# Optimization experiments

Measured on AMD Instinct MI355X. Metric: run time of the kernel, lower is better.

The kernel has to match this reference:

```python
import jax, jax.numpy as jnp
import numpy as np

N, E, D, R, L = 100000, 800000, 64, 7, 3
HID, KH = D // 4, 32          # IEConv hidden = dims[i]//4, kernel_hidden_dim = 32
EDGE_DIM = 14
BN_EPS = 1e-5
LN_EPS = 1e-5


def _normalize(v, eps=1e-12):
    n = jnp.linalg.norm(v, axis=-1, keepdims=True)
    return v / jnp.maximum(n, eps)


def _bn(h, p):
    # eval-mode BatchNorm1d; p: [4, dim] = (gamma, beta, running_mean, running_var)
    return (h - p[2]) * jax.lax.rsqrt(p[3] + BN_EPS) * p[0] + p[1]


def setup_inputs() -> dict:
    key = jax.random.key(0)
    keys = iter(jax.random.split(key, 40))
    nk = lambda: next(keys)
    par = lambda shape, s=0.1: jax.random.normal(nk(), shape, jnp.float32) * s

    def bn_par(dim):
        g = 1.0 + 0.1 * jax.random.normal(nk(), (L, dim), jnp.float32)
        b = 0.1 * jax.random.normal(nk(), (L, dim), jnp.float32)
        m = 0.1 * jax.random.normal(nk(), (L, dim), jnp.float32)
        v = 0.5 + jax.random.uniform(nk(), (L, dim), jnp.float32)
        return jnp.stack([g, b, m, v], axis=1)  # [L,4,dim]

    inp = {
        "x": jax.random.normal(nk(), (N, D), jnp.float32),
        "pos": jax.random.normal(nk(), (N, 3), jnp.float32) * 10.0,
        "edge_index": jax.random.randint(nk(), (2, E), 0, N),
        "edge_relation": jax.random.randint(nk(), (E,), 0, R),
        # GeometricRelationalGraphConv params (per layer)
        "W_rel": par((L, R * D, D)), "b_rel": par((L, D)),
        "W_self": par((L, D, D)), "b_self": par((L, D)),
        # IEConvLayer params
        "W_l1": par((L, D, HID)), "b_l1": par((L, HID)),
        "W_k1": par((L, EDGE_DIM, KH)), "b_k1": par((L, KH)),
        "W_k2": par((L, KH, (HID + 1) * HID)), "b_k2": par((L, (HID + 1) * HID)),
        "W_l2": par((L, HID, D)), "b_l2": par((L, D)),
        "bn_in": bn_par(D), "bn_msg": bn_par(HID), "bn_upd": bn_par(HID), "bn_out": bn_par(D),
        "ln_g": 1.0 + 0.1 * jax.random.normal(nk(), (L, D), jnp.float32),
        "ln_b": 0.1 * jax.random.normal(nk(), (L, D), jnp.float32),
    }
    return inp


def _forward(x, pos, W_rel, b_rel, W_self, b_self, W_l1, b_l1, W_k1, b_k1,
             W_k2, b_k2, W_l2, b_l2, bn_in, bn_msg, bn_upd, bn_out, ln_g, ln_b,
             edge_index, edge_relation):
    node_in, node_out = edge_index[0], edge_index[1]
    # ---- get_ieconv_edge_feature ----
    ones3 = jnp.ones((1, 3), x.dtype)
    u = _normalize(jnp.concatenate([ones3, pos[1:] - pos[:-1]], axis=0))        # [N,3]
    b = _normalize(jnp.concatenate([u[:-1] - u[1:], ones3], axis=0))
    n = _normalize(jnp.concatenate([jnp.cross(u[:-1], u[1:]), ones3], axis=0))
    frame = jnp.stack([b, n, jnp.cross(b, n)], axis=-1)                          # [N,3,3]
    t = jnp.einsum('ejk,ej->ek', frame[node_in], pos[node_out] - pos[node_in])  # [E,3]
    r = jnp.sum(frame[node_in] * frame[node_out], axis=1)                        # [E,3]
    delta = (jnp.abs(node_in - node_out).astype(x.dtype) / 6.0)[:, None]         # atom2residue = arange
    edge_feat = jnp.concatenate(
        [t, r, delta, 1 - 2 * jnp.abs(t), 1 - 2 * jnp.abs(r), 1 - 2 * jnp.abs(delta)], axis=-1)  # [E,14]

    deg = jnp.maximum(
        jax.ops.segment_sum(jnp.ones_like(node_out, dtype=x.dtype), node_out, num_segments=N), 1.0)[:, None]
    seg = node_out * R + edge_relation
    h = x
    for i in range(L):
        # GeometricRelationalGraphConv: relation-bucketed scatter-sum, per-relation linear + self loop, relu
        upd = jax.ops.segment_sum(h[node_in], seg, num_segments=N * R).reshape(N, R * h.shape[-1])
        rel_out = jax.nn.relu(upd @ W_rel[i] + b_rel[i] + h @ W_self[i] + b_self[i])
        # IEConvLayer (eval mode, dropouts identity)
        li = jax.nn.relu(_bn(h, bn_in[i]))
        m = jax.nn.relu(_bn(li[node_in] @ W_l1[i] + b_l1[i], bn_msg[i]))         # [E,HID]
        ker = (jax.nn.relu(edge_feat @ W_k1[i] + b_k1[i]) @ W_k2[i] + b_k2[i]).reshape(-1, HID + 1, HID)
        m = jnp.einsum('ejk,ej->ek', ker[:, 1:, :], m) + ker[:, 0, :]            # per-edge kernel conv
        upd2 = jax.ops.segment_sum(m, node_out, num_segments=N) / deg            # scatter-mean
        upd2 = jax.nn.relu(_bn(upd2, bn_upd[i]))
        ie_out = _bn(upd2 @ W_l2[i] + b_l2[i], bn_out[i])
        hidden = rel_out + ie_out + h  # short_cut: shapes match at every layer
        mu = jnp.mean(hidden, axis=-1, keepdims=True)
        var = jnp.var(hidden, axis=-1, keepdims=True)
        h = (hidden - mu) * jax.lax.rsqrt(var + LN_EPS) * ln_g[i] + ln_b[i]
    return h


def reference(x, pos, edge_index, edge_relation, W_rel, b_rel, W_self, b_self,
              W_l1, b_l1, W_k1, b_k1, W_k2, b_k2, W_l2, b_l2,
              bn_in, bn_msg, bn_upd, bn_out, ln_g, ln_b):
    return _forward(x, pos, W_rel, b_rel, W_self, b_self, W_l1, b_l1, W_k1, b_k1,
                    W_k2, b_k2, W_l2, b_l2, bn_in, bn_msg, bn_upd, bn_out, ln_g, ln_b,
                    edge_index, edge_relation)
```

## Files before the change

### kernel.cpp

```cpp
#include <hip/hip_runtime.h>
#include <hip/hip_bf16.h>

typedef unsigned short u16;
typedef unsigned int   u32;

static const int Nn  = 100000;
static const int Ne  = 800000;
static const int Ll  = 3;
static const int SCAN_B = 98;

typedef short     short8  __attribute__((ext_vector_type(8)));
typedef float     floatx4 __attribute__((ext_vector_type(4)));

static const int H_CUM[19] = {
  0, 86016, 86208, 98496, 98688, 101760, 101808, 103152, 103248,
  129360, 130176, 133248, 133440, 134208, 134400, 134592, 135360, 135552, 135744
};
static const int H_SZ[18] = {
  86016, 192, 12288, 192, 3072, 48, 1344, 96,
  26112, 816, 3072, 192, 768, 192, 192, 768, 192, 192
};

union FU { u32 u; float f; };
__device__ __forceinline__ float b2f(u16 v) { FU x; x.u = ((u32)v) << 16; return x.f; }
__device__ __forceinline__ float lo2f(u32 w) { FU x; x.u = w << 16; return x.f; }
__device__ __forceinline__ float hi2f(u32 w) { FU x; x.u = w & 0xffff0000u; return x.f; }
__device__ __forceinline__ u16 f2b(float f) {
  FU x; x.f = f;
  u32 u = x.u;
  u32 r = (u + 0x7FFFu + ((u >> 16) & 1u)) >> 16;
  return (u16)r;
}
__device__ __forceinline__ u32 pk2(float a, float b) {
  __hip_bfloat162 h2 = __float22bfloat162_rn(make_float2(a, b));
  union { __hip_bfloat162 h; u32 u; } c; c.h = h2; return c.u;
}

__global__ void k_bnprep(const float* __restrict__ W, float* __restrict__ bnAB) {
  int idx = blockIdx.x * blockDim.x + threadIdx.x;
  if (idx >= 480) return;
  int i = idx / 160, d0 = idx % 160;
  const float* src; float* dstA; float* dstB; int dim, d;
  if (d0 < 64)       { d = d0;      src = W + 133440 + i * 256; dim = 64; dstA = bnAB + i*320 + 0;   dstB = bnAB + i*320 + 64;  }
  else if (d0 < 80)  { d = d0 - 64; src = W + 134208 + i * 64;  dim = 16; dstA = bnAB + i*320 + 128; dstB = bnAB + i*320 + 144; }
  else if (d0 < 96)  { d = d0 - 80; src = W + 134400 + i * 64;  dim = 16; dstA = bnAB + i*320 + 160; dstB = bnAB + i*320 + 176; }
  else               { d = d0 - 96; src = W + 134592 + i * 256; dim = 64; dstA = bnAB + i*320 + 192; dstB = bnAB + i*320 + 256; }
  float g = src[0*dim+d], b = src[1*dim+d], m = src[2*dim+d], v = src[3*dim+d];
  float A = g * rsqrtf(v + 1e-5f);
  float B = b - m * A;
  dstA[d] = A; dstB[d] = B;
}

__global__ void k_prep(const float* __restrict__ W, u16* __restrict__ BswG) {
  int i = blockIdx.x * 256 + threadIdx.x;
  if (i >= 3 * 8704) return;
  int layer = i / 8704, r = i % 8704;
  int jp = r / 512, l2 = r % 512;
  int lane = l2 / 8, j = l2 % 8;
  int q = (lane >> 4) * 8 + j, n = lane & 15;
  const float* Wk2 = W + 103248 + layer * 8704;
  BswG[i] = f2b(Wk2[q * 272 + jp * 16 + n]);
}

__global__ void k_prep2(const float* __restrict__ W, u16* __restrict__ B2) {
  int idx = blockIdx.x * 256 + threadIdx.x;
  if (idx >= 3 * 65536) return;
  int layer = idx >> 16, r = idx & 65535;
  int fr = r >> 9;
  int lane = (r >> 3) & 63, j = r & 7;
  int hl = fr & 1, ks = (fr >> 1) & 1, nt = (fr >> 2) & 3, nc = fr >> 4;
  int k = ks * 32 + (lane >> 4) * 8 + j;
  int g = nc * 64 + nt * 16 + (lane & 15);
  const float* Wrel  = W + layer * 28672;
  const float* Wself = W + 86208 + layer * 4096;
  float v = (g < 448) ? Wrel[((g >> 6) * 64 + k) * 64 + (g & 63)]
                      : Wself[k * 64 + (g - 448)];
  u16 hi = f2b(v);
  B2[idx] = hl ? f2b(v - b2f(hi)) : hi;
}

__global__ void k_prep3(const float* __restrict__ W, u16* __restrict__ Wk1f) {
  int idx = blockIdx.x * 256 + threadIdx.x;
  if (idx >= 3 * 2048) return;
  int layer = idx / 2048, r = idx % 2048;
  int kind = (r >> 10) & 1, nt = (r >> 9) & 1;
  int lane = (r >> 3) & 63, j = r & 7;
  int k = (lane >> 4) * 8 + j;
  int q = nt * 16 + (lane & 15);
  const float* Wk1 = W + 101808 + layer * 448;
  u16 out = 0;
  if (kind == 0) {
    if (k < 14)       out = f2b(Wk1[k * 32 + q]);
    else if (k < 28)  out = f2b(Wk1[(k - 14) * 32 + q]);
  } else {
    if (k < 14) {
      float w = Wk1[k * 32 + q];
      u16 hi = f2b(w);
      out = f2b(w - b2f(hi));
    }
  }
  Wk1f[idx] = out;
}

__global__ void k_u(const float* __restrict__ posf, float* __restrict__ u) {
  int i = blockIdx.x * blockDim.x + threadIdx.x;
  if (i >= Nn) return;
  float ux, uy, uz;
  if (i == 0) { ux = uy = uz = 0.57735026918962584f; }
  else {
    float vx = posf[i*3+0] - posf[(i-1)*3+0];
    float vy = posf[i*3+1] - posf[(i-1)*3+1];
    float vz = posf[i*3+2] - posf[(i-1)*3+2];
    float nrm = sqrtf(vx*vx + vy*vy + vz*vz);
    float inv = 1.0f / fmaxf(nrm, 1e-12f);
    ux = vx*inv; uy = vy*inv; uz = vz*inv;
  }
  u[i*3+0] = ux; u[i*3+1] = uy; u[i*3+2] = uz;
}

__global__ void k_frame(const float* __restrict__ u, float* __restrict__ frame) {
  int i = blockIdx.x * blockDim.x + threadIdx.x;
  if (i >= Nn) return;
  float bx, by, bz, nx, ny, nz;
  if (i < Nn - 1) {
    float ax = u[i*3+0], ay = u[i*3+1], az = u[i*3+2];
    float cx = u[(i+1)*3+0], cy = u[(i+1)*3+1], cz = u[(i+1)*3+2];
    float dx = ax-cx, dy = ay-cy, dz = az-cz;
    float n1 = sqrtf(dx*dx + dy*dy + dz*dz);
    float i1 = 1.0f / fmaxf(n1, 1e-12f);
    bx = dx*i1; by = dy*i1; bz = dz*i1;
    float qx = ay*cz - az*cy, qy = az*cx - ax*cz, qz = ax*cy - ay*cx;
    float n2 = sqrtf(qx*qx + qy*qy + qz*qz);
    float i2 = 1.0f / fmaxf(n2, 1e-12f);
    nx = qx*i2; ny = qy*i2; nz = qz*i2;
  } else {
    bx = by = bz = 0.57735026918962584f;
    nx = ny = nz = 0.57735026918962584f;
  }
  float ex = by*nz - bz*ny, ey = bz*nx - bx*nz, ez = bx*ny - by*nx;
  frame[i*9+0] = bx; frame[i*9+1] = nx; frame[i*9+2] = ex;
  frame[i*9+3] = by; frame[i*9+4] = ny; frame[i*9+5] = ey;
  frame[i*9+6] = bz; frame[i*9+7] = nz; frame[i*9+8] = ez;
}

__global__ void k_edge(const int* __restrict__ EI, const float* __restrict__ posf,
                       const float* __restrict__ frame,
                       float* __restrict__ t0, float* __restrict__ t1, float* __restrict__ t2,
                       float* __restrict__ r0, float* __restrict__ r1, float* __restrict__ r2,
                       int* __restrict__ cnt) {
  int e = blockIdx.x * 256 + threadIdx.x;
  int vin = EI[e], vout = EI[Ne + e];
  float fi[9], fo[9];
#pragma unroll
  for (int t = 0; t < 9; t++) fi[t] = frame[(size_t)vin*9 + t];
#pragma unroll
  for (int t = 0; t < 9; t++) fo[t] = frame[(size_t)vout*9 + t];
  float d0 = posf[vout*3+0] - posf[vin*3+0];
  float d1 = posf[vout*3+1] - posf[vin*3+1];
  float d2 = posf[vout*3+2] - posf[vin*3+2];
  float tt[3], rr[3];
#pragma unroll
  for (int k = 0; k < 3; k++) {
    tt[k] = fi[0*3+k]*d0 + fi[1*3+k]*d1 + fi[2*3+k]*d2;
    rr[k] = fi[0*3+k]*fo[0*3+k] + fi[1*3+k]*fo[1*3+k] + fi[2*3+k]*fo[2*3+k];
  }
  t0[e] = tt[0]; t1[e] = tt[1]; t2[e] = tt[2];
  r0[e] = rr[0]; r1[e] = rr[1]; r2[e] = rr[2];
  atomicAdd(&cnt[vout], 1);
}

__global__ __launch_bounds__(1024) void k_scan1(const int* __restrict__ cnt,
                                                int* __restrict__ locExc,
                                                int* __restrict__ btot) {
  __shared__ int sm[1024];
  int t = threadIdx.x, b = blockIdx.x;
  int i = b * 1024 + t;
  int v = (i < Nn) ? cnt[i] : 0;
  sm[t] = v;
  __syncthreads();
#pragma unroll
  for (int off = 1; off < 1024; off <<= 1) {
    int x = (t >= off) ? sm[t - off] : 0;
    __syncthreads();
    sm[t] += x;
    __syncthreads();
  }
  if (i < Nn) locExc[i] = sm[t] - v;
  if (t == 1023) btot[b] = sm[1023];
}

__global__ void k_scan2(const int* __restrict__ btot, int* __restrict__ boff,
                        int* __restrict__ rowptr) {
  if (threadIdx.x != 0 || blockIdx.x != 0) return;
  int run = 0;
  for (int b = 0; b < SCAN_B; b++) { boff[b] = run; run += btot[b]; }
  rowptr[Nn] = run;
}

__global__ void k_scan3(const int* __restrict__ cnt, const int* __restrict__ locExc,
                        const int* __restrict__ boff, int* __restrict__ rowptr,
                        float* __restrict__ deginv) {
  int i = blockIdx.x * blockDim.x + threadIdx.x;
  if (i >= Nn) return;
  rowptr[i] = locExc[i] + boff[i >> 10];
  int dv = cnt[i] > 1 ? cnt[i] : 1;
  deginv[i] = 1.0f / (float)dv;
}

__global__ void k_place(const int* __restrict__ EI, const int* __restrict__ EREL,
                        const int* __restrict__ rowptr,
                        int* __restrict__ fill, int* __restrict__ yidx,
                        int* __restrict__ inv) {
  int e = blockIdx.x * blockDim.x + threadIdx.x;
  if (e >= Ne) return;
  int vout = EI[Ne + e];
  int p = atomicAdd(&fill[vout], 1);
  int slot = rowptr[vout] + p;
  inv[e] = slot;
  yidx[slot] = EI[e] * 448 + EREL[e] * 64;
}

__global__ __launch_bounds__(256) void k_rel2(
    const float* __restrict__ h, const u16* __restrict__ Bsw,
    const float* __restrict__ brel, const float* __restrict__ bself,
    u16* __restrict__ Y, u16* __restrict__ S) {
  __shared__ uint4 bs4[1024];
  int tid = threadIdx.x;
  int w = tid >> 6, lane = tid & 63;
  int kq = lane >> 4, cl = lane & 15;
  int nb0 = blockIdx.x * 64;
  int anode = nb0 + w * 16 + cl;
  union U { uint4 u; short8 v; };

  uint4 Ah[2], Al[2];
#pragma unroll
  for (int ks = 0; ks < 2; ks++) {
    float p[8] = {0.f,0.f,0.f,0.f,0.f,0.f,0.f,0.f};
    if (anode < Nn) {
      const float4* hp = (const float4*)(h + (size_t)anode * 64 + ks * 32 + kq * 8);
      float4 q0 = hp[0], q1 = hp[1];
      p[0]=q0.x; p[1]=q0.y; p[2]=q0.z; p[3]=q0.w;
      p[4]=q1.x; p[5]=q1.y; p[6]=q1.z; p[7]=q1.w;
    }
    u32 hw[4], lw[4];
#pragma unroll
    for (int t = 0; t < 4; t++) {
      u16 ha = f2b(p[2*t]), hb = f2b(p[2*t+1]);
      hw[t] = (u32)ha | ((u32)hb << 16);
      lw[t] = pk2(p[2*t] - b2f(ha), p[2*t+1] - b2f(hb));
    }
    Ah[ks] = make_uint4(hw[0], hw[1], hw[2], hw[3]);
    Al[ks] = make_uint4(lw[0], lw[1], lw[2], lw[3]);
  }

  for (int nc = 0; nc < 8; nc++) {
    if (nc) __syncthreads();
    const uint4* src = (const uint4*)(Bsw + nc * 8192);
#pragma unroll
    for (int i = 0; i < 4; i++) bs4[tid + i * 256] = src[tid + i * 256];
    __syncthreads();

    floatx4 acc[4];
#pragma unroll
    for (int nt = 0; nt < 4; nt++) acc[nt] = (floatx4){0.f, 0.f, 0.f, 0.f};
#pragma unroll
    for (int nt = 0; nt < 4; nt++) {
#pragma unroll
      for (int ks = 0; ks < 2; ks++) {
        U bh, bl, ah, al;
        bh.u = bs4[((nt*2 + ks)*2 + 0)*64 + lane];
        bl.u = bs4[((nt*2 + ks)*2 + 1)*64 + lane];
        ah.u = Ah[ks]; al.u = Al[ks];
        acc[nt] = __builtin_amdgcn_mfma_f32_16x16x32_bf16(ah.v, bh.v, acc[nt], 0, 0, 0);
        acc[nt] = __builtin_amdgcn_mfma_f32_16x16x32_bf16(al.v, bh.v, acc[nt], 0, 0, 0);
        acc[nt] = __builtin_amdgcn_mfma_f32_16x16x32_bf16(ah.v, bl.v, acc[nt], 0, 0, 0);
      }
    }
    if (nc < 7) {
#pragma unroll
      for (int nt = 0; nt < 4; nt++) {
#pragma unroll
        for (int reg = 0; reg < 4; reg++) {
          int node = nb0 + w * 16 + kq * 4 + reg;
          if (node < Nn)
            Y[(size_t)node * 448 + nc * 64 + nt * 16 + cl] = f2b(acc[nt][reg]);
        }
      }
    } else {
#pragma unroll
      for (int nt = 0; nt < 4; nt++) {
        int c = nt * 16 + cl;
        float bias = brel[c] + bself[c];
#pragma unroll
        for (int reg = 0; reg < 4; reg++) {
          int node = nb0 + w * 16 + kq * 4 + reg;
          if (node < Nn)
            S[(size_t)node * 64 + c] = f2b(acc[nt][reg] + bias);
        }
      }
    }
  }
}

__global__ __launch_bounds__(256) void k_z(
    const float* __restrict__ h, const float* __restrict__ Wl1, const float* __restrict__ bl1,
    const float* __restrict__ bk2, const float* __restrict__ bn,
    u16* __restrict__ zt, u16* __restrict__ biast) {
  __shared__ float ls[64][65];
  __shared__ float zz[64][17];
  int tid = threadIdx.x;
  int nb0 = blockIdx.x * 64;
  const float* Ain = bn + 0;
  const float* Bin = bn + 64;
#pragma unroll
  for (int r = 0; r < 16; r++) {
    int idx = r * 256 + tid;
    int row = idx >> 6, col = idx & 63;
    int node = nb0 + row;
    float v = (node < Nn) ? h[(size_t)node * 64 + col] : 0.0f;
    ls[row][col] = fmaxf(v * Ain[col] + Bin[col], 0.0f);
  }
  __syncthreads();
  int row = tid >> 2, jq = (tid & 3) * 4;
  int node = nb0 + row;
  const float* Amsg = bn + 128;
  const float* Bmsg = bn + 144;
  float m1[4];
#pragma unroll
  for (int t = 0; t < 4; t++) m1[t] = bl1[jq + t];
  for (int c = 0; c < 64; c++) {
    float lv = ls[row][c];
#pragma unroll
    for (int t = 0; t < 4; t++) m1[t] += lv * Wl1[c * 16 + jq + t];
  }
  float zv[4];
#pragma unroll
  for (int t = 0; t < 4; t++) {
    zv[t] = fmaxf(m1[t] * Amsg[jq + t] + Bmsg[jq + t], 0.0f);
    zz[row][jq + t] = zv[t];
  }
  if (node < Nn) {
    u32* zg = (u32*)zt + (size_t)node * 8 + (tid & 3) * 2;
    zg[0] = pk2(zv[0], zv[1]);
    zg[1] = pk2(zv[2], zv[3]);
  }
  __syncthreads();
  float bb[4];
#pragma unroll
  for (int t = 0; t < 4; t++) bb[t] = bk2[jq + t];
  for (int j = 0; j < 16; j++) {
    float zj = zz[row][j];
#pragma unroll
    for (int t = 0; t < 4; t++) bb[t] += zj * bk2[(j + 1) * 16 + jq + t];
  }
  if (node < Nn) {
    u32* bg = (u32*)biast + (size_t)node * 8 + (tid & 3) * 2;
    bg[0] = pk2(bb[0], bb[1]);
    bg[1] = pk2(bb[2], bb[3]);
  }
}

__global__ __launch_bounds__(256) void k_msg(
    const float* __restrict__ t0, const float* __restrict__ t1, const float* __restrict__ t2,
    const float* __restrict__ r0, const float* __restrict__ r1, const float* __restrict__ r2,
    const int* __restrict__ EI, const int* __restrict__ inv,
    const u16* __restrict__ zt, const u16* __restrict__ biast,
    const u16* __restrict__ Wk1f, const float* __restrict__ bk1,
    const u16* __restrict__ BswG, u16* __restrict__ mo) {
  __shared__ u16 abuf[256 * 40];
  __shared__ int ivin[256];

  int tid = threadIdx.x;
  int e0 = blockIdx.x * 256;
  int e = e0 + tid;

  int vin = EI[e], vout = EI[Ne + e];
  ivin[tid] = vin;

  float ef[14];
  ef[0] = t0[e]; ef[1] = t1[e]; ef[2] = t2[e];
  ef[3] = r0[e]; ef[4] = r1[e]; ef[5] = r2[e];
  int ad = vin - vout; if (ad < 0) ad = -ad;
  ef[6] = ((float)ad) / 6.0f;
#pragma unroll
  for (int k = 0; k < 7; k++) ef[7+k] = 1.0f - 2.0f*fabsf(ef[k]);

  u16 row[32];
#pragma unroll
  for (int d = 0; d < 14; d++) {
    u16 hi = f2b(ef[d]);
    row[d] = hi;
    row[14 + d] = f2b(ef[d] - b2f(hi));
  }
#pragma unroll
  for (int d = 28; d < 32; d++) row[d] = 0;
  u32* ar = (u32*)(abuf + (size_t)tid * 40);
#pragma unroll
  for (int i = 0; i < 16; i++)
    ar[i] = (u32)row[2*i] | ((u32)row[2*i+1] << 16);
  __syncthreads();

  int lane = tid & 63, w4 = (tid >> 6) * 4;
  int m = lane & 15, quad = lane >> 4;
  union U { uint4 u; short8 v; };

  U b0[2], b1[2];
#pragma unroll
  for (int nt = 0; nt < 2; nt++) {
    b0[nt].u = *(const uint4*)(Wk1f + 0*1024 + nt*512 + lane*8);
    b1[nt].u = *(const uint4*)(Wk1f + 1*1024 + nt*512 + lane*8);
  }
  float bk1v[2] = { bk1[m], bk1[16 + m] };
  const u16* bswL = BswG + (size_t)lane * 8;

#pragma unroll
  for (int t = 0; t < 4; t++) {
    int s0 = (w4 + t) * 16;
    const u16* rs0 = abuf + (size_t)(s0 + m) * 40;

    U efr; efr.u = *(const uint4*)(rs0 + quad * 8);
#pragma unroll
    for (int nt = 0; nt < 2; nt++) {
      floatx4 aa = {0.f, 0.f, 0.f, 0.f};
      aa = __builtin_amdgcn_mfma_f32_16x16x32_bf16(efr.v, b0[nt].v, aa, 0, 0, 0);
      aa = __builtin_amdgcn_mfma_f32_16x16x32_bf16(efr.v, b1[nt].v, aa, 0, 0, 0);
#pragma unroll
      for (int reg = 0; reg < 4; reg++) {
        int se = s0 + quad * 4 + reg;
        float av = fmaxf(aa[reg] + bk1v[nt], 0.0f);
        abuf[(size_t)se * 40 + nt * 16 + m] = f2b(av);
      }
    }
    U afr; afr.u = *(const uint4*)(rs0 + quad * 8);

    int se0 = s0 + quad * 4;
    uint4 z0[4], z1[4]; float bv[4]; int sl[4];
#pragma unroll
    for (int reg = 0; reg < 4; reg++) {
      int vi = ivin[se0 + reg];
      const uint4* zp = (const uint4*)(zt + (size_t)vi * 16);
      z0[reg] = zp[0]; z1[reg] = zp[1];
      bv[reg] = b2f(biast[(size_t)vi * 16 + m]);
      sl[reg] = inv[e0 + se0 + reg];
    }

    float acc[4];
    {
      U bfr; bfr.u = *(const uint4*)(bswL);
      floatx4 zz4 = {0.f, 0.f, 0.f, 0.f};
      floatx4 k0 = __builtin_amdgcn_mfma_f32_16x16x32_bf16(afr.v, bfr.v, zz4, 0, 0, 0);
#pragma unroll
      for (int reg = 0; reg < 4; reg++) acc[reg] = k0[reg];
    }
#pragma unroll
    for (int jp = 1; jp <= 16; jp++) {
      U bfr; bfr.u = *(const uint4*)(bswL + (size_t)jp * 512);
      floatx4 zz4 = {0.f, 0.f, 0.f, 0.f};
      floatx4 kj = __builtin_amdgcn_mfma_f32_16x16x32_bf16(afr.v, bfr.v, zz4, 0, 0, 0);
      const int zi = jp - 1;
#pragma unroll
      for (int reg = 0; reg < 4; reg++) {
        const u32* zw = (zi < 8) ? (const u32*)&z0[reg] : (const u32*)&z1[reg];
        u32 wv = zw[(zi & 7) >> 1];
        float zv = (zi & 1) ? hi2f(wv) : lo2f(wv);
        acc[reg] += zv * kj[reg];
      }
    }
#pragma unroll
    for (int reg = 0; reg < 4; reg++)
      mo[(size_t)sl[reg] * 16 + m] = f2b(acc[reg] + bv[reg]);
  }
}

__global__ __launch_bounds__(256) void k_node(
    const float* __restrict__ h, const u16* __restrict__ S, const u16* __restrict__ Y,
    const int* __restrict__ rowptr, const int* __restrict__ yidx,
    const u16* __restrict__ mo, const float* __restrict__ deginv,
    const float* __restrict__ Wl2, const float* __restrict__ bl2,
    const float* __restrict__ bn, const float* __restrict__ lng, const float* __restrict__ lnb,
    float* __restrict__ hout) {
  __shared__ float relsm[4][64];
  __shared__ float u2s[4][16];
  int tid = threadIdx.x;
  int lane = tid & 63, w = tid >> 6;
  int n = blockIdx.x * 4 + w;
  bool act = (n < Nn);

  if (act) {
    int beg = rowptr[n], end = rowptr[n+1];

    int g = lane >> 4, col4 = lane & 15;
    float a4[4] = {0.f, 0.f, 0.f, 0.f};
    for (int c0 = beg; c0 < end; c0 += 64) {
      int l = c0 + lane;
      int yo = (l < end) ? yidx[l] : 0;
      int cnt = end - c0; if (cnt > 64) cnt = 64;
      for (int j0 = 0; j0 < cnt; j0 += 8) {
        int jA = j0 + g;
        int jB = j0 + 4 + g;
        int yA = __shfl(yo, jA, 64);
        int yB = __shfl(yo, jB, 64);
        bool vA = (jA < cnt), vB = (jB < cnt);
        uint2 dA = vA ? *(const uint2*)(Y + (size_t)yA + col4 * 4) : make_uint2(0u, 0u);
        uint2 dB = vB ? *(const uint2*)(Y + (size_t)yB + col4 * 4) : make_uint2(0u, 0u);
        a4[0] += lo2f(dA.x); a4[1] += hi2f(dA.x);
        a4[2] += lo2f(dA.y); a4[3] += hi2f(dA.y);
        a4[0] += lo2f(dB.x); a4[1] += hi2f(dB.x);
        a4[2] += lo2f(dB.y); a4[3] += hi2f(dB.y);
      }
    }
#pragma unroll
    for (int t = 0; t < 4; t++) {
      a4[t] += __shfl_xor(a4[t], 16, 64);
      a4[t] += __shfl_xor(a4[t], 32, 64);
    }
    if (lane < 16) {
#pragma unroll
      for (int t = 0; t < 4; t++) relsm[w][col4 * 4 + t] = a4[t];
    }

    int r = lane >> 2, c4 = lane & 3;
    float p4[4] = {0.f, 0.f, 0.f, 0.f};
    for (int p0 = beg; p0 < end; p0 += 16) {
      int p = p0 + r;
      if (p < end) {
        uint2 d = *(const uint2*)(mo + (size_t)p * 16 + c4 * 4);
        p4[0] += lo2f(d.x); p4[1] += hi2f(d.x);
        p4[2] += lo2f(d.y); p4[3] += hi2f(d.y);
      }
    }
#pragma unroll
    for (int t = 0; t < 4; t++) {
      p4[t] += __shfl_xor(p4[t],  4, 64);
      p4[t] += __shfl_xor(p4[t],  8, 64);
      p4[t] += __shfl_xor(p4[t], 16, 64);
      p4[t] += __shfl_xor(p4[t], 32, 64);
    }
    const float* Aupd = bn + 160;
    const float* Bupd = bn + 176;
    if (lane < 4) {
      float di = deginv[n];
#pragma unroll
      for (int t = 0; t < 4; t++) {
        int col = c4 * 4 + t;
        float v = p4[t] * di;
        u2s[w][col] = fmaxf(v * Aupd[col] + Bupd[col], 0.0f);
      }
    }
  }
  __syncthreads();
  if (act) {
    float rel_out = fmaxf(b2f(S[(size_t)n*64 + lane]) + relsm[w][lane], 0.0f);
    float ie = bl2[lane];
#pragma unroll
    for (int j = 0; j < 16; j++) ie += u2s[w][j] * Wl2[j*64 + lane];
    const float* Aout = bn + 192;
    const float* Bout = bn + 256;
    ie = ie * Aout[lane] + Bout[lane];
    float hidden = rel_out + ie + h[(size_t)n*64 + lane];
    float s = hidden;
#pragma unroll
    for (int off = 32; off > 0; off >>= 1) s += __shfl_xor(s, off, 64);
    float mu = s * (1.0f/64.0f);
    float d = hidden - mu;
    float s2 = d * d;
#pragma unroll
    for (int off = 32; off > 0; off >>= 1) s2 += __shfl_xor(s2, off, 64);
    float var = s2 * (1.0f/64.0f);
    float o = d * rsqrtf(var + 1e-5f) * lng[lane] + lnb[lane];
    hout[(size_t)n*64 + lane] = o;
  }
}

extern "C" void kernel_launch(void* const* d_in, const int* in_sizes, int n_in,
                              void* d_out, int out_size, void* d_ws, size_t ws_size,
                              hipStream_t stream) {
  const float* x    = (const float*)d_in[0];
  const float* posf = (const float*)d_in[1];
  const int* EI     = (const int*)d_in[2];
  const int* EREL   = (const int*)d_in[3];
  float* outf       = (float*)d_out;

  char* p = (char*)d_ws;
  auto alloc = [&](size_t bytes) -> char* {
    char* r = p;
    p += (bytes + 255) & ~((size_t)255);
    return r;
  };
  float* W      = (float*)alloc((size_t)135744 * 4);
  float* bnAB   = (float*)alloc((size_t)960 * 4);
  u16*   BswG   = (u16*)  alloc((size_t)3 * 8704 * 2);
  u16*   Bsw2   = (u16*)  alloc((size_t)3 * 65536 * 2);
  u16*   Wk1f   = (u16*)  alloc((size_t)3 * 2048 * 2);
  float* u      = (float*)alloc((size_t)Nn * 3 * 4);
  float* frame  = (float*)alloc((size_t)Nn * 9 * 4);
  int*   cnt    = (int*)  alloc((size_t)Nn * 4);
  int*   fill   = (int*)  alloc((size_t)Nn * 4);
  int*   rowptr = (int*)  alloc((size_t)(Nn + 1) * 4);
  int*   locExc = (int*)  alloc((size_t)Nn * 4);
  int*   btot   = (int*)  alloc((size_t)SCAN_B * 4);
  int*   boff   = (int*)  alloc((size_t)SCAN_B * 4);
  int*   yidx   = (int*)  alloc((size_t)Ne * 4);
  int*   inv    = (int*)  alloc((size_t)Ne * 4);
  float* deginv = (float*)alloc((size_t)Nn * 4);
  float* h      = (float*)alloc((size_t)Nn * 64 * 4);
  u16*   S      = (u16*)  alloc((size_t)Nn * 64 * 2);
  u16*   Y      = (u16*)  alloc((size_t)Nn * 448 * 2);
  u16*   mo     = (u16*)  alloc((size_t)Ne * 16 * 2);
  u16*   zt     = (u16*)  alloc((size_t)Nn * 16 * 2);
  u16*   biast  = (u16*)  alloc((size_t)Nn * 16 * 2);
  float* et0    = (float*)alloc((size_t)Ne * 4);
  float* et1    = (float*)alloc((size_t)Ne * 4);
  float* et2    = (float*)alloc((size_t)Ne * 4);
  float* er0    = (float*)alloc((size_t)Ne * 4);
  float* er1    = (float*)alloc((size_t)Ne * 4);
  float* er2    = (float*)alloc((size_t)Ne * 4);
  (void)n_in; (void)in_sizes; (void)out_size;

  size_t needed = (size_t)(p - (char*)d_ws);
  if (needed > ws_size) return;

  hipMemsetAsync(cnt,  0, (size_t)Nn * 4, stream);
  hipMemsetAsync(fill, 0, (size_t)Nn * 4, stream);

  for (int k = 0; k < 18; k++)
    hipMemcpyAsync(W + H_CUM[k], d_in[4 + k], (size_t)H_SZ[k] * 4,
                   hipMemcpyDeviceToDevice, stream);
  hipMemcpyAsync(h, x, (size_t)Nn * 64 * 4, hipMemcpyDeviceToDevice, stream);

  k_bnprep<<<2, 256, 0, stream>>>(W, bnAB);
  k_prep<<<(3*8704 + 255)/256, 256, 0, stream>>>(W, BswG);
  k_prep2<<<(3*65536 + 255)/256, 256, 0, stream>>>(W, Bsw2);
  k_prep3<<<(3*2048 + 255)/256, 256, 0, stream>>>(W, Wk1f);
  k_u<<<(Nn + 255)/256, 256, 0, stream>>>(posf, u);
  k_frame<<<(Nn + 255)/256, 256, 0, stream>>>(u, frame);
  k_edge<<<Ne/256, 256, 0, stream>>>(EI, posf, frame, et0, et1, et2, er0, er1, er2, cnt);
  k_scan1<<<SCAN_B, 1024, 0, stream>>>(cnt, locExc, btot);
  k_scan2<<<1, 64, 0, stream>>>(btot, boff, rowptr);
  k_scan3<<<(Nn + 255)/256, 256, 0, stream>>>(cnt, locExc, boff, rowptr, deginv);
  k_place<<<Ne/256, 256, 0, stream>>>(EI, EREL, rowptr, fill, yidx, inv);

  for (int i = 0; i < Ll; i++) {
    const float* brel  = W + H_CUM[1]  + i * 64;
    const float* bself = W + H_CUM[3]  + i * 64;
    const float* Wl1   = W + H_CUM[4]  + i * 1024;
    const float* bl1   = W + H_CUM[5]  + i * 16;
    const float* bk1   = W + H_CUM[7]  + i * 32;
    const float* bk2   = W + H_CUM[9]  + i * 272;
    const float* Wl2   = W + H_CUM[10] + i * 1024;
    const float* bl2   = W + H_CUM[11] + i * 64;
    const float* lng   = W + H_CUM[16] + i * 64;
    const float* lnb   = W + H_CUM[17] + i * 64;
    const float* bnL   = bnAB + i * 320;
    const u16*   BswL  = BswG + i * 8704;

    k_rel2<<<(Nn + 63)/64, 256, 0, stream>>>(h, Bsw2 + i * 65536, brel, bself, Y, S);
    k_z<<<(Nn + 63)/64, 256, 0, stream>>>(h, Wl1, bl1, bk2, bnL, zt, biast);
    k_msg<<<Ne/256, 256, 0, stream>>>(et0, et1, et2, er0, er1, er2, EI, inv,
                                      zt, biast, Wk1f + i * 2048, bk1, BswL, mo);
    k_node<<<(Nn + 3)/4, 256, 0, stream>>>(h, S, Y, rowptr, yidx, mo, deginv,
                                           Wl2, bl2, bnL, lng, lnb,
                                           (i == Ll - 1) ? outf : h);
  }
}
```

Baseline: 794.6 us.

## Replace per-edge message buffer with atomic float scatter into per-node accumulator

New measurement: 802.4 us. No clear change (+1.0%).

```diff
diff --git a/kernel.cpp b/kernel.cpp
--- a/kernel.cpp
+++ b/kernel.cpp
@@ -209,14 +209,12 @@
 
 __global__ void k_place(const int* __restrict__ EI, const int* __restrict__ EREL,
                         const int* __restrict__ rowptr,
-                        int* __restrict__ fill, int* __restrict__ yidx,
-                        int* __restrict__ inv) {
+                        int* __restrict__ fill, int* __restrict__ yidx) {
   int e = blockIdx.x * blockDim.x + threadIdx.x;
   if (e >= Ne) return;
   int vout = EI[Ne + e];
   int p = atomicAdd(&fill[vout], 1);
   int slot = rowptr[vout] + p;
-  inv[e] = slot;
   yidx[slot] = EI[e] * 448 + EREL[e] * 64;
 }
 
@@ -363,12 +361,13 @@
 __global__ __launch_bounds__(256) void k_msg(
     const float* __restrict__ t0, const float* __restrict__ t1, const float* __restrict__ t2,
     const float* __restrict__ r0, const float* __restrict__ r1, const float* __restrict__ r2,
-    const int* __restrict__ EI, const int* __restrict__ inv,
+    const int* __restrict__ EI,
     const u16* __restrict__ zt, const u16* __restrict__ biast,
     const u16* __restrict__ Wk1f, const float* __restrict__ bk1,
-    const u16* __restrict__ BswG, u16* __restrict__ mo) {
+    const u16* __restrict__ BswG, float* __restrict__ moacc) {
   __shared__ u16 abuf[256 * 40];
   __shared__ int ivin[256];
+  __shared__ int ivout[256];
 
   int tid = threadIdx.x;
   int e0 = blockIdx.x * 256;
@@ -376,6 +375,7 @@
 
   int vin = EI[e], vout = EI[Ne + e];
   ivin[tid] = vin;
+  ivout[tid] = vout;
 
   float ef[14];
   ef[0] = t0[e]; ef[1] = t1[e]; ef[2] = t2[e];
@@ -434,14 +434,14 @@
     U afr; afr.u = *(const uint4*)(rs0 + quad * 8);
 
     int se0 = s0 + quad * 4;
-    uint4 z0[4], z1[4]; float bv[4]; int sl[4];
+    uint4 z0[4], z1[4]; float bv[4]; int vo[4];
 #pragma unroll
     for (int reg = 0; reg < 4; reg++) {
       int vi = ivin[se0 + reg];
       const uint4* zp = (const uint4*)(zt + (size_t)vi * 16);
       z0[reg] = zp[0]; z1[reg] = zp[1];
       bv[reg] = b2f(biast[(size_t)vi * 16 + m]);
-      sl[reg] = inv[e0 + se0 + reg];
+      vo[reg] = ivout[se0 + reg];
     }
 
     float acc[4];
@@ -468,14 +468,14 @@
     }
 #pragma unroll
     for (int reg = 0; reg < 4; reg++)
-      mo[(size_t)sl[reg] * 16 + m] = f2b(acc[reg] + bv[reg]);
+      atomicAdd(&moacc[(size_t)vo[reg] * 16 + m], acc[reg] + bv[reg]);
   }
 }
 
 __global__ __launch_bounds__(256) void k_node(
     const float* __restrict__ h, const u16* __restrict__ S, const u16* __restrict__ Y,
     const int* __restrict__ rowptr, const int* __restrict__ yidx,
-    const u16* __restrict__ mo, const float* __restrict__ deginv,
+    const float* __restrict__ moacc, const float* __restrict__ deginv,
     const float* __restrict__ Wl2, const float* __restrict__ bl2,
     const float* __restrict__ bn, const float* __restrict__ lng, const float* __restrict__ lnb,
     float* __restrict__ hout) {
@@ -519,33 +519,11 @@
       for (int t = 0; t < 4; t++) relsm[w][col4 * 4 + t] = a4[t];
     }
 
-    int r = lane >> 2, c4 = lane & 3;
-    float p4[4] = {0.f, 0.f, 0.f, 0.f};
-    for (int p0 = beg; p0 < end; p0 += 16) {
-      int p = p0 + r;
-      if (p < end) {
-        uint2 d = *(const uint2*)(mo + (size_t)p * 16 + c4 * 4);
-        p4[0] += lo2f(d.x); p4[1] += hi2f(d.x);
-        p4[2] += lo2f(d.y); p4[3] += hi2f(d.y);
-      }
-    }
-#pragma unroll
-    for (int t = 0; t < 4; t++) {
-      p4[t] += __shfl_xor(p4[t],  4, 64);
-      p4[t] += __shfl_xor(p4[t],  8, 64);
-      p4[t] += __shfl_xor(p4[t], 16, 64);
-      p4[t] += __shfl_xor(p4[t], 32, 64);
-    }
     const float* Aupd = bn + 160;
     const float* Bupd = bn + 176;
-    if (lane < 4) {
-      float di = deginv[n];
-#pragma unroll
-      for (int t = 0; t < 4; t++) {
-        int col = c4 * 4 + t;
-        float v = p4[t] * di;
-        u2s[w][col] = fmaxf(v * Aupd[col] + Bupd[col], 0.0f);
-      }
+    if (lane < 16) {
+      float v = moacc[(size_t)n * 16 + lane] * deginv[n];
+      u2s[w][lane] = fmaxf(v * Aupd[lane] + Bupd[lane], 0.0f);
     }
   }
   __syncthreads();
@@ -601,12 +579,11 @@
   int*   btot   = (int*)  alloc((size_t)SCAN_B * 4);
   int*   boff   = (int*)  alloc((size_t)SCAN_B * 4);
   int*   yidx   = (int*)  alloc((size_t)Ne * 4);
-  int*   inv    = (int*)  alloc((size_t)Ne * 4);
   float* deginv = (float*)alloc((size_t)Nn * 4);
   float* h      = (float*)alloc((size_t)Nn * 64 * 4);
   u16*   S      = (u16*)  alloc((size_t)Nn * 64 * 2);
   u16*   Y      = (u16*)  alloc((size_t)Nn * 448 * 2);
-  u16*   mo     = (u16*)  alloc((size_t)Ne * 16 * 2);
+  float* moacc  = (float*)alloc((size_t)Nn * 16 * 4);
   u16*   zt     = (u16*)  alloc((size_t)Nn * 16 * 2);
   u16*   biast  = (u16*)  alloc((size_t)Nn * 16 * 2);
   float* et0    = (float*)alloc((size_t)Ne * 4);
@@ -638,7 +615,7 @@
   k_scan1<<<SCAN_B, 1024, 0, stream>>>(cnt, locExc, btot);
   k_scan2<<<1, 64, 0, stream>>>(btot, boff, rowptr);
   k_scan3<<<(Nn + 255)/256, 256, 0, stream>>>(cnt, locExc, boff, rowptr, deginv);
-  k_place<<<Ne/256, 256, 0, stream>>>(EI, EREL, rowptr, fill, yidx, inv);
+  k_place<<<Ne/256, 256, 0, stream>>>(EI, EREL, rowptr, fill, yidx);
 
   for (int i = 0; i < Ll; i++) {
     const float* brel  = W + H_CUM[1]  + i * 64;
@@ -654,11 +631,12 @@
     const float* bnL   = bnAB + i * 320;
     const u16*   BswL  = BswG + i * 8704;
 
+    hipMemsetAsync(moacc, 0, (size_t)Nn * 16 * 4, stream);
     k_rel2<<<(Nn + 63)/64, 256, 0, stream>>>(h, Bsw2 + i * 65536, brel, bself, Y, S);
     k_z<<<(Nn + 63)/64, 256, 0, stream>>>(h, Wl1, bl1, bk2, bnL, zt, biast);
-    k_msg<<<Ne/256, 256, 0, stream>>>(et0, et1, et2, er0, er1, er2, EI, inv,
-                                      zt, biast, Wk1f + i * 2048, bk1, BswL, mo);
-    k_node<<<(Nn + 3)/4, 256, 0, stream>>>(h, S, Y, rowptr, yidx, mo, deginv,
+    k_msg<<<Ne/256, 256, 0, stream>>>(et0, et1, et2, er0, er1, er2, EI,
+                                      zt, biast, Wk1f + i * 2048, bk1, BswL, moacc);
+    k_node<<<(Nn + 3)/4, 256, 0, stream>>>(h, S, Y, rowptr, yidx, moacc, deginv,
                                            Wl2, bl2, bnL, lng, lnb,
                                            (i == Ll - 1) ? outf : h);
   }
```
